# Optimization experiments

Hardware: AMD Instinct MI355X
Metric: run time of the kernel (lower is better)

The kernel has to match this reference:

```python
import jax, jax.numpy as jnp
import numpy as np

TOP_K = 2  # top-k experts per token


def setup_inputs() -> dict:
    key = jax.random.key(0)
    k1, k2, k3, k4, k5 = jax.random.split(key, 5)
    B, S, D = 1, 2048, 2048
    E, F = 8, 1408
    scale = 0.02
    return {
        "hidden_states": jax.random.normal(k1, (B, S, D), dtype=jnp.float32),
        "gate_w": jax.random.normal(k2, (E, D), dtype=jnp.float32) * scale,
        "w_gate": jax.random.normal(k3, (E, D, F), dtype=jnp.float32) * scale,
        "w_up": jax.random.normal(k4, (E, D, F), dtype=jnp.float32) * scale,
        "w_down": jax.random.normal(k5, (E, F, D), dtype=jnp.float32) * scale,
    }


def reference(hidden_states, gate_w, w_gate, w_up, w_down):
    B, S, D = hidden_states.shape
    T = B * S
    x = hidden_states.reshape(T, D)  # flatten tokens, as in forward()

    # Router: combined gate built from per-rank 1-row gates -> [T, E] logits
    router_logits = jnp.einsum("td,ed->te", x, gate_w)
    routing_weights = jax.nn.softmax(router_logits, axis=-1)
    top_w, top_idx = jax.lax.top_k(routing_weights, TOP_K)  # [T, K]

    # Per-token combine weight for each expert (0 if expert not selected).
    # Equivalent to the one_hot expert_mask + index_add combine in the module.
    comb = jnp.zeros((T, gate_w.shape[0]), dtype=routing_weights.dtype)
    comb = comb.at[jnp.arange(T)[:, None], top_idx].add(top_w)  # [T, E]

    # Each expert is a Qwen2 MLP: down(silu(gate(x)) * up(x)).
    # (Dispatch/all-to-all collapses to dense-per-expert + masked combine
    #  on a single device; tokens with comb==0 contribute nothing.)
    g = jnp.einsum("td,edf->etf", x, w_gate)
    u = jnp.einsum("td,edf->etf", x, w_up)
    y = jnp.einsum("etf,efd->etd", jax.nn.silu(g) * u, w_down)  # [E, T, D]

    out = jnp.einsum("te,etd->td", comb, y)  # weighted combine (index_add)
    return out.reshape(B, S, D)
```

## Files before the change

kernel.cpp:

```cpp
#include <hip/hip_runtime.h>
#include <stdint.h>


#define TT 2048
#define DD 2048
#define FF 1408
#define NE 8
#define HROWS 5120
#define TRASH (2*TT)

typedef float f32x4 __attribute__((ext_vector_type(4)));
typedef short bf16x8 __attribute__((ext_vector_type(8)));
typedef short bf16x4 __attribute__((ext_vector_type(4)));
typedef const __attribute__((address_space(3))) unsigned short* lds_cp;

__device__ __forceinline__ unsigned short f2bf(float f) {
    unsigned int x = __float_as_uint(f);
    return (unsigned short)((x + 0x7fffu + ((x >> 16) & 1u)) >> 16);
}
__device__ __forceinline__ float bf2f(unsigned short u) {
    union { unsigned int i; float f; } v; v.i = ((unsigned int)u) << 16; return v.f;
}
__device__ __forceinline__ void gld16(const void* g, void* l) {
    __builtin_amdgcn_global_load_lds((const __attribute__((address_space(1))) void*)g,
                                     (__attribute__((address_space(3))) void*)l, 16, 0, 0);
}

#define TR16(d, p, imm) \
    asm volatile("ds_read_b64_tr_b16 %0, %1 offset:" imm : "=&v"(d) : "v"(p))

__global__ void convert_gu_kernel(const float* __restrict__ wg,
                                  const float* __restrict__ wu,
                                  unsigned short* __restrict__ G,
                                  unsigned short* __restrict__ U) {
    const int z = blockIdx.z;
    const float* s; unsigned short* d;
    if (z < NE) { s = wg + (size_t)z * DD * FF;        d = G + (size_t)z * DD * FF; }
    else        { s = wu + (size_t)(z - NE) * DD * FF; d = U + (size_t)(z - NE) * DD * FF; }
    const size_t i = ((size_t)blockIdx.x * 256 + threadIdx.x) * 8;
    float4 a = *(const float4*)(s + i);
    float4 b = *(const float4*)(s + i + 4);
    uint4 o; unsigned short* po = (unsigned short*)&o;
    po[0] = f2bf(a.x); po[1] = f2bf(a.y); po[2] = f2bf(a.z); po[3] = f2bf(a.w);
    po[4] = f2bf(b.x); po[5] = f2bf(b.y); po[6] = f2bf(b.z); po[7] = f2bf(b.w);
    *(uint4*)(d + i) = o;
}

__global__ void convert_d_kernel(const float* __restrict__ wd,
                                 unsigned short* __restrict__ W) {
    const int z = blockIdx.z;
    const float* s = wd + (size_t)z * FF * DD;
    unsigned short* d = W + (size_t)z * FF * DD;
    const size_t i = ((size_t)blockIdx.x * 256 + threadIdx.x) * 8;
    float4 a = *(const float4*)(s + i);
    float4 b = *(const float4*)(s + i + 4);
    uint4 o; unsigned short* po = (unsigned short*)&o;
    po[0] = f2bf(a.x); po[1] = f2bf(a.y); po[2] = f2bf(a.z); po[3] = f2bf(a.w);
    po[4] = f2bf(b.x); po[5] = f2bf(b.y); po[6] = f2bf(b.z); po[7] = f2bf(b.w);
    *(uint4*)(d + i) = o;
}

__global__ void router_kernel(const float* __restrict__ x,
                              const float* __restrict__ gw,
                              int* __restrict__ cnt,
                              int* __restrict__ tok,
                              float* __restrict__ wtv,
                              int* __restrict__ dstv,
                              unsigned short* __restrict__ xb,
                              int* __restrict__ basep,
                              int* __restrict__ cntpad) {
    __shared__ int s_last;
    __shared__ int sc[NE], sp[NE];

    const int wv = threadIdx.x >> 6, lane = threadIdx.x & 63;
    const int t = blockIdx.x * 4 + wv;
    float acc[NE];
#pragma unroll
    for (int e = 0; e < NE; ++e) acc[e] = 0.f;
    const float* xr = x + (size_t)t * DD;
    unsigned short* xbr = xb + (size_t)t * DD;
#pragma unroll
    for (int it = 0; it < DD / 256; ++it) {
        const int j = it * 256 + lane * 4;
        float4 xv = *(const float4*)(xr + j);
        short4 o;
        o.x = (short)f2bf(xv.x); o.y = (short)f2bf(xv.y);
        o.z = (short)f2bf(xv.z); o.w = (short)f2bf(xv.w);
        *(short4*)(xbr + j) = o;
#pragma unroll
        for (int e = 0; e < NE; ++e) {
            float4 g = *(const float4*)(gw + e * DD + j);
            acc[e] += xv.x * g.x + xv.y * g.y + xv.z * g.z + xv.w * g.w;
        }
    }
#pragma unroll
    for (int e = 0; e < NE; ++e) {
        float v = acc[e];
        v += __shfl_xor(v, 32); v += __shfl_xor(v, 16); v += __shfl_xor(v, 8);
        v += __shfl_xor(v, 4);  v += __shfl_xor(v, 2);  v += __shfl_xor(v, 1);
        acc[e] = v;
    }
    if (lane == 0) {
        float mx = acc[0];
#pragma unroll
        for (int e = 1; e < NE; ++e) mx = fmaxf(mx, acc[e]);
        float p[NE], s = 0.f;
#pragma unroll
        for (int e = 0; e < NE; ++e) { p[e] = __expf(acc[e] - mx); s += p[e]; }
        int i0 = 0;
#pragma unroll
        for (int e = 1; e < NE; ++e) if (p[e] > p[i0]) i0 = e;
        int i1 = (i0 == 0) ? 1 : 0;
#pragma unroll
        for (int e = 0; e < NE; ++e) if (e != i0 && p[e] > p[i1]) i1 = e;
        float inv = 1.f / s;
        int p0 = atomicAdd(&cnt[i0], 1);
        tok[i0 * TT + p0] = t; wtv[i0 * TT + p0] = p[i0] * inv; dstv[i0 * TT + p0] = 2 * t;
        int p1 = atomicAdd(&cnt[i1], 1);
        tok[i1 * TT + p1] = t; wtv[i1 * TT + p1] = p[i1] * inv; dstv[i1 * TT + p1] = 2 * t + 1;
    }

    __syncthreads();
    if (threadIdx.x == 0) {
        __threadfence();
        int d = atomicAdd(&cnt[NE], 1);
        s_last = (d == (TT / 4) - 1) ? 1 : 0;
    }
    __syncthreads();
    if (s_last) {
        if (threadIdx.x == 0) {
            int b = 0;
            for (int e = 0; e < NE; ++e) {
                int c = atomicAdd(&cnt[e], 0);
                int pd = (c + 127) & ~127;
                basep[e] = b; cntpad[e] = pd; sc[e] = c; sp[e] = pd; b += pd;
            }
        }
        __syncthreads();
        for (int e = 0; e < NE; ++e)
            for (int i = sc[e] + (int)threadIdx.x; i < sp[e]; i += 256) {
                tok[e * TT + i] = 0; wtv[e * TT + i] = 0.f; dstv[e * TT + i] = TRASH;
            }
    }
}


__launch_bounds__(256, 2)
__global__ void gemm1_kernel(const unsigned short* __restrict__ Xb,
                             const unsigned short* __restrict__ Wg,
                             const unsigned short* __restrict__ Wu,
                             const int* __restrict__ tok,
                             const int* __restrict__ base,
                             const int* __restrict__ cntpad,
                             unsigned short* __restrict__ H) {
    __shared__ unsigned short As[128 * 32];
    __shared__ unsigned short Bg[128 * 32];
    __shared__ unsigned short Bu[128 * 32];
    __shared__ int s_tok[128];

    const int e = blockIdx.z, rb = blockIdx.y, fb = blockIdx.x;
    const int cp = cntpad[e];
    if (rb * 128 >= cp) return;
    const int b0 = base[e];

    const int tid = threadIdx.x;
    if (tid < 128) s_tok[tid] = tok[e * TT + rb * 128 + tid];
    __syncthreads();

    const int w = tid >> 6, lane = tid & 63;
    const int r = lane & 15, q = lane >> 4;
    const int wm = w & 1, wn = w >> 1;

    const int srow = w * 32 + (lane >> 2);
    const int koff = (lane & 3) * 8;
    const unsigned short* ga0 = Xb + (size_t)s_tok[srow] * DD + koff;
    const unsigned short* ga1 = Xb + (size_t)s_tok[srow + 16] * DD + koff;
    unsigned short* la0 = As + srow * 32 + koff;
    unsigned short* la1 = la0 + 512;

    const int s0 = tid, s1 = tid + 256;
    const int k0 = 4 * (s0 >> 6) + ((s0 >> 1) & 3), f0 = 16 * ((s0 >> 3) & 7) + 8 * (s0 & 1);
    const int k1 = 4 * (s1 >> 6) + ((s1 >> 1) & 3), f1 = 16 * ((s1 >> 3) & 7) + 8 * (s1 & 1);
    const size_t wb = (size_t)e * DD * FF + (size_t)fb * 128;
    const unsigned short* gg0 = Wg + wb + (size_t)k0 * FF + f0;
    const unsigned short* gg1 = Wg + wb + (size_t)k1 * FF + f1;
    const unsigned short* gu0 = Wu + wb + (size_t)k0 * FF + f0;
    const unsigned short* gu1 = Wu + wb + (size_t)k1 * FF + f1;
    unsigned short* lg0 = Bg + s0 * 8;
    unsigned short* lg1 = Bg + s1 * 8;
    unsigned short* lu0 = Bu + s0 * 8;
    unsigned short* lu1 = Bu + s1 * 8;

    lds_cp bg = (lds_cp)Bg + (q * 1024 + wn * 256 + 4 * r);
    lds_cp bu = (lds_cp)Bu + (q * 1024 + wn * 256 + 4 * r);

    f32x4 accg[4][4] = {};
    f32x4 accu[4][4] = {};

    for (int kt = 0; kt < DD / 32; ++kt) {
        gld16(ga0, la0); gld16(ga1, la1);
        gld16(gg0, lg0); gld16(gg1, lg1);
        gld16(gu0, lu0); gld16(gu1, lu1);
        ga0 += 32; ga1 += 32;
        gg0 += 32 * FF; gg1 += 32 * FF; gu0 += 32 * FF; gu1 += 32 * FF;
        __syncthreads();

        bf16x8 af[4];
#pragma unroll
        for (int m = 0; m < 4; ++m)
            af[m] = *(const bf16x8*)&As[(wm * 64 + m * 16 + r) * 32 + q * 8];

        bf16x4 gA[8], uA[8];
        TR16(gA[0], bg, "0");    TR16(gA[1], bg, "1024");
        TR16(gA[2], bg, "128");  TR16(gA[3], bg, "1152");
        TR16(gA[4], bg, "256");  TR16(gA[5], bg, "1280");
        TR16(gA[6], bg, "384");  TR16(gA[7], bg, "1408");
        TR16(uA[0], bu, "0");    TR16(uA[1], bu, "1024");
        TR16(uA[2], bu, "128");  TR16(uA[3], bu, "1152");
        TR16(uA[4], bu, "256");  TR16(uA[5], bu, "1280");
        TR16(uA[6], bu, "384");  TR16(uA[7], bu, "1408");
        asm volatile("s_waitcnt lgkmcnt(0)" ::: "memory");
        __builtin_amdgcn_sched_barrier(0);

        bf16x8 gf[4], uf[4];
#pragma unroll
        for (int n = 0; n < 4; ++n) {
            gf[n] = __builtin_shufflevector(gA[2 * n], gA[2 * n + 1], 0, 1, 2, 3, 4, 5, 6, 7);
            uf[n] = __builtin_shufflevector(uA[2 * n], uA[2 * n + 1], 0, 1, 2, 3, 4, 5, 6, 7);
        }
#pragma unroll
        for (int m = 0; m < 4; ++m)
#pragma unroll
            for (int n = 0; n < 4; ++n) {
                accg[m][n] = __builtin_amdgcn_mfma_f32_16x16x32_bf16(af[m], gf[n], accg[m][n], 0, 0, 0);
                accu[m][n] = __builtin_amdgcn_mfma_f32_16x16x32_bf16(af[m], uf[n], accu[m][n], 0, 0, 0);
            }
        __syncthreads();
    }

    const size_t hr0 = (size_t)(b0 + rb * 128 + wm * 64);
#pragma unroll
    for (int m = 0; m < 4; ++m)
#pragma unroll
        for (int n = 0; n < 4; ++n)
#pragma unroll
            for (int rr = 0; rr < 4; ++rr) {
                float g = accg[m][n][rr], u = accu[m][n][rr];
                float h = (g / (1.f + __expf(-g))) * u;
                int row = m * 16 + q * 4 + rr;
                int col = fb * 128 + wn * 64 + n * 16 + r;
                H[(hr0 + row) * FF + col] = f2bf(h);
            }
}

__launch_bounds__(256, 2)
__global__ void gemm2_kernel(const unsigned short* __restrict__ H,
                             const unsigned short* __restrict__ Wd,
                             const float* __restrict__ wtv,
                             const int* __restrict__ dstv,
                             const int* __restrict__ base,
                             const int* __restrict__ cntpad,
                             unsigned short* __restrict__ Y) {
    __shared__ unsigned short As[128 * 32];
    __shared__ unsigned short Bs[128 * 32];
    __shared__ float s_w[128];
    __shared__ int s_d[128];

    const int e = blockIdx.z, rb = blockIdx.y, db = blockIdx.x;
    const int cp = cntpad[e];
    if (rb * 128 >= cp) return;
    const int b0 = base[e];

    const int tid = threadIdx.x;
    if (tid < 128) {
        int idx = e * TT + rb * 128 + tid;
        s_w[tid] = wtv[idx]; s_d[tid] = dstv[idx];
    }
    __syncthreads();

    const int w = tid >> 6, lane = tid & 63;
    const int r = lane & 15, q = lane >> 4;
    const int wm = w & 1, wn = w >> 1;

    const int srow = w * 32 + (lane >> 2);
    const int koff = (lane & 3) * 8;
    const unsigned short* ga0 = H + (size_t)(b0 + rb * 128 + srow) * FF + koff;
    const unsigned short* ga1 = ga0 + (size_t)16 * FF;
    unsigned short* la0 = As + srow * 32 + koff;
    unsigned short* la1 = la0 + 512;

    const int s0 = tid, s1 = tid + 256;
    const int k0 = 4 * (s0 >> 6) + ((s0 >> 1) & 3), f0 = 16 * ((s0 >> 3) & 7) + 8 * (s0 & 1);
    const int k1 = 4 * (s1 >> 6) + ((s1 >> 1) & 3), f1 = 16 * ((s1 >> 3) & 7) + 8 * (s1 & 1);
    const size_t wb = (size_t)e * FF * DD + (size_t)db * 128;
    const unsigned short* gb0 = Wd + wb + (size_t)k0 * DD + f0;
    const unsigned short* gb1 = Wd + wb + (size_t)k1 * DD + f1;
    unsigned short* lb0 = Bs + s0 * 8;
    unsigned short* lb1 = Bs + s1 * 8;

    lds_cp bb = (lds_cp)Bs + (q * 1024 + wn * 256 + 4 * r);

    f32x4 acc[4][4] = {};

    for (int kt = 0; kt < FF / 32; ++kt) {
        gld16(ga0, la0); gld16(ga1, la1);
        gld16(gb0, lb0); gld16(gb1, lb1);
        ga0 += 32; ga1 += 32;
        gb0 += 32 * DD; gb1 += 32 * DD;
        __syncthreads();

        bf16x8 af[4];
#pragma unroll
        for (int m = 0; m < 4; ++m)
            af[m] = *(const bf16x8*)&As[(wm * 64 + m * 16 + r) * 32 + q * 8];

        bf16x4 bA[8];
        TR16(bA[0], bb, "0");    TR16(bA[1], bb, "1024");
        TR16(bA[2], bb, "128");  TR16(bA[3], bb, "1152");
        TR16(bA[4], bb, "256");  TR16(bA[5], bb, "1280");
        TR16(bA[6], bb, "384");  TR16(bA[7], bb, "1408");
        asm volatile("s_waitcnt lgkmcnt(0)" ::: "memory");
        __builtin_amdgcn_sched_barrier(0);

        bf16x8 bf[4];
#pragma unroll
        for (int n = 0; n < 4; ++n)
            bf[n] = __builtin_shufflevector(bA[2 * n], bA[2 * n + 1], 0, 1, 2, 3, 4, 5, 6, 7);
#pragma unroll
        for (int m = 0; m < 4; ++m)
#pragma unroll
            for (int n = 0; n < 4; ++n)
                acc[m][n] = __builtin_amdgcn_mfma_f32_16x16x32_bf16(af[m], bf[n], acc[m][n], 0, 0, 0);
        __syncthreads();
    }

#pragma unroll
    for (int m = 0; m < 4; ++m)
#pragma unroll
        for (int n = 0; n < 4; ++n)
#pragma unroll
            for (int rr = 0; rr < 4; ++rr) {
                int row = wm * 64 + m * 16 + q * 4 + rr;
                int col = db * 128 + wn * 64 + n * 16 + r;
                float v = s_w[row] * acc[m][n][rr];
                Y[(size_t)s_d[row] * DD + col] = f2bf(v);
            }
}

__global__ void combine_kernel(const unsigned short* __restrict__ Y,
                               float* __restrict__ out) {
    const int t = blockIdx.x;
    const int d = threadIdx.x * 8;
    uint4 a = *(const uint4*)(Y + (size_t)(2 * t) * DD + d);
    uint4 b = *(const uint4*)(Y + (size_t)(2 * t + 1) * DD + d);
    const unsigned short* pa = (const unsigned short*)&a;
    const unsigned short* pb = (const unsigned short*)&b;
    float4 o0, o1;
    o0.x = bf2f(pa[0]) + bf2f(pb[0]);  o0.y = bf2f(pa[1]) + bf2f(pb[1]);
    o0.z = bf2f(pa[2]) + bf2f(pb[2]);  o0.w = bf2f(pa[3]) + bf2f(pb[3]);
    o1.x = bf2f(pa[4]) + bf2f(pb[4]);  o1.y = bf2f(pa[5]) + bf2f(pb[5]);
    o1.z = bf2f(pa[6]) + bf2f(pb[6]);  o1.w = bf2f(pa[7]) + bf2f(pb[7]);
    float* op = out + (size_t)t * DD + d;
    ((float4*)op)[0] = o0;
    ((float4*)op)[1] = o1;
}

extern "C" void kernel_launch(void* const* d_in, const int* in_sizes, int n_in,
                              void* d_out, int out_size, void* d_ws, size_t ws_size,
                              hipStream_t stream) {
    const float* x      = (const float*)d_in[0];
    const float* gw     = (const float*)d_in[1];
    const float* w_gate = (const float*)d_in[2];
    const float* w_up   = (const float*)d_in[3];
    const float* w_down = (const float*)d_in[4];
    float* out = (float*)d_out;

    uint8_t* ws = (uint8_t*)d_ws;
    size_t off = 0;
    auto alloc = [&](size_t bytes) -> void* {
        void* p = ws + off;
        off = (off + bytes + 255) & ~(size_t)255;
        return p;
    };
    int*   cnt    = (int*)  alloc((NE + 1) * 4);
    int*   basep  = (int*)  alloc(NE * 4);
    int*   cntpad = (int*)  alloc(NE * 4);
    int*   tok    = (int*)  alloc((size_t)NE * TT * 4);
    float* wtv    = (float*)alloc((size_t)NE * TT * 4);
    int*   dstv   = (int*)  alloc((size_t)NE * TT * 4);
    unsigned short* Xb  = (unsigned short*)alloc((size_t)TT * DD * 2);
    unsigned short* Hb  = (unsigned short*)alloc((size_t)HROWS * FF * 2);
    unsigned short* Yb  = (unsigned short*)alloc((size_t)(2 * TT + 8) * DD * 2);
    unsigned short* WT  = (unsigned short*)alloc((size_t)2 * NE * FF * DD * 2);
    unsigned short* WgB = WT;
    unsigned short* WuB = WT + (size_t)NE * FF * DD;
    unsigned short* WdB = WT;
    (void)ws_size; (void)in_sizes; (void)n_in; (void)out_size;

    hipMemsetAsync(cnt, 0, (NE + 1) * 4, stream);
    convert_gu_kernel<<<dim3(DD * FF / 2048, 1, 2 * NE), 256, 0, stream>>>(w_gate, w_up, WgB, WuB);
    router_kernel<<<dim3(TT / 4), 256, 0, stream>>>(x, gw, cnt, tok, wtv, dstv, Xb, basep, cntpad);
    gemm1_kernel<<<dim3(FF / 128, TT / 128, NE), 256, 0, stream>>>(Xb, WgB, WuB, tok, basep, cntpad, Hb);
    convert_d_kernel<<<dim3(FF * DD / 2048, 1, NE), 256, 0, stream>>>(w_down, WdB);
    gemm2_kernel<<<dim3(DD / 128, TT / 128, NE), 256, 0, stream>>>(Hb, WdB, wtv, dstv, basep, cntpad, Yb);
    combine_kernel<<<dim3(TT), 256, 0, stream>>>(Yb, out);
}
```

Measured before the change: 497.6 us.

## Double-buffer LDS tiles in both expert GEMMs and remap block order

Both grouped GEMM kernels now keep two LDS buffers and issue the next K-tile's global-to-LDS loads before computing on the current one. Explicit vmcnt waits and raw s_barrier calls replace the per-iteration __syncthreads, so memory latency can overlap the MFMA work. Block indices are also permuted so that consecutively launched blocks are spread across row and column tiles, which changes how weight tiles are reused in cache. LDS use per block doubles, which could reduce occupancy, and the hand-written wait counts must match the number of loads in flight or the results will be wrong.

Result: slower. 666.9 us (+34.0%).

```diff
diff --git a/kernel.cpp b/kernel.cpp
--- a/kernel.cpp
+++ b/kernel.cpp
@@ -28,6 +28,9 @@
 
 #define TR16(d, p, imm) \
     asm volatile("ds_read_b64_tr_b16 %0, %1 offset:" imm : "=&v"(d) : "v"(p))
+
+#define WAITV(n)  asm volatile("s_waitcnt vmcnt(" #n ")" ::: "memory")
+#define BARRIER() asm volatile("s_barrier" ::: "memory")
 
 __global__ void convert_gu_kernel(const float* __restrict__ wg,
                                   const float* __restrict__ wu,
@@ -144,6 +147,50 @@
     }
 }
 
+#define G1_STAGE(BUF) do {                                                     \
+    gld16(ga0, &As[BUF][a_s0]); gld16(ga1, &As[BUF][a_s1]);                    \
+    gld16(gg0, &Bg[BUF][b_s0]); gld16(gg1, &Bg[BUF][b_s1]);                    \
+    gld16(gu0, &Bu[BUF][b_s0]); gld16(gu1, &Bu[BUF][b_s1]);                    \
+    ga0 += 32; ga1 += 32;                                                      \
+    gg0 += 32 * FF; gg1 += 32 * FF; gu0 += 32 * FF; gu1 += 32 * FF;            \
+} while (0)
+
+#define G1_COMPUTE(BUF) do {                                                   \
+    bf16x8 af[4];                                                              \
+    af[0] = *(const bf16x8*)&As[BUF][ar0];                                     \
+    af[1] = *(const bf16x8*)&As[BUF][ar0 + 512];                               \
+    af[2] = *(const bf16x8*)&As[BUF][ar0 + 1024];                              \
+    af[3] = *(const bf16x8*)&As[BUF][ar0 + 1536];                              \
+    bf16x4 gA[8], uA[8];                                                       \
+    {                                                                          \
+        lds_cp bgp = (lds_cp)(&Bg[BUF][0]) + boff;                             \
+        lds_cp bup = (lds_cp)(&Bu[BUF][0]) + boff;                             \
+        TR16(gA[0], bgp, "0");    TR16(gA[1], bgp, "1024");                    \
+        TR16(gA[2], bgp, "128");  TR16(gA[3], bgp, "1152");                    \
+        TR16(gA[4], bgp, "256");  TR16(gA[5], bgp, "1280");                    \
+        TR16(gA[6], bgp, "384");  TR16(gA[7], bgp, "1408");                    \
+        TR16(uA[0], bup, "0");    TR16(uA[1], bup, "1024");                    \
+        TR16(uA[2], bup, "128");  TR16(uA[3], bup, "1152");                    \
+        TR16(uA[4], bup, "256");  TR16(uA[5], bup, "1280");                    \
+        TR16(uA[6], bup, "384");  TR16(uA[7], bup, "1408");                    \
+    }                                                                          \
+    asm volatile("s_waitcnt lgkmcnt(0)" ::: "memory");                         \
+    __builtin_amdgcn_sched_barrier(0);                                         \
+    bf16x8 gf[4], uf[4];                                                       \
+    _Pragma("unroll")                                                          \
+    for (int n = 0; n < 4; ++n) {                                              \
+        gf[n] = __builtin_shufflevector(gA[2*n], gA[2*n+1], 0,1,2,3,4,5,6,7);  \
+        uf[n] = __builtin_shufflevector(uA[2*n], uA[2*n+1], 0,1,2,3,4,5,6,7);  \
+    }                                                                          \
+    _Pragma("unroll")                                                          \
+    for (int m = 0; m < 4; ++m) {                                              \
+        _Pragma("unroll")                                                      \
+        for (int n = 0; n < 4; ++n) {                                          \
+            accg[m][n] = __builtin_amdgcn_mfma_f32_16x16x32_bf16(af[m], gf[n], accg[m][n], 0, 0, 0); \
+            accu[m][n] = __builtin_amdgcn_mfma_f32_16x16x32_bf16(af[m], uf[n], accu[m][n], 0, 0, 0); \
+        }                                                                      \
+    }                                                                          \
+} while (0)
 
 __launch_bounds__(256, 2)
 __global__ void gemm1_kernel(const unsigned short* __restrict__ Xb,
@@ -153,12 +200,16 @@
                              const int* __restrict__ base,
                              const int* __restrict__ cntpad,
                              unsigned short* __restrict__ H) {
-    __shared__ unsigned short As[128 * 32];
-    __shared__ unsigned short Bg[128 * 32];
-    __shared__ unsigned short Bu[128 * 32];
+    __shared__ unsigned short As[2][128 * 32];
+    __shared__ unsigned short Bg[2][128 * 32];
+    __shared__ unsigned short Bu[2][128 * 32];
     __shared__ int s_tok[128];
 
-    const int e = blockIdx.z, rb = blockIdx.y, fb = blockIdx.x;
+    const int e = blockIdx.z;
+    const int u = blockIdx.y * 11 + blockIdx.x;
+    const int wk = 22 * (u & 7) + (u >> 3);
+    const int rb = wk / 11, fb = wk % 11;
+
     const int cp = cntpad[e];
     if (rb * 128 >= cp) return;
     const int b0 = base[e];
@@ -175,8 +226,7 @@
     const int koff = (lane & 3) * 8;
     const unsigned short* ga0 = Xb + (size_t)s_tok[srow] * DD + koff;
     const unsigned short* ga1 = Xb + (size_t)s_tok[srow + 16] * DD + koff;
-    unsigned short* la0 = As + srow * 32 + koff;
-    unsigned short* la1 = la0 + 512;
+    const int a_s0 = srow * 32 + koff, a_s1 = a_s0 + 512;
 
     const int s0 = tid, s1 = tid + 256;
     const int k0 = 4 * (s0 >> 6) + ((s0 >> 1) & 3), f0 = 16 * ((s0 >> 3) & 7) + 8 * (s0 & 1);
@@ -186,56 +236,30 @@
     const unsigned short* gg1 = Wg + wb + (size_t)k1 * FF + f1;
     const unsigned short* gu0 = Wu + wb + (size_t)k0 * FF + f0;
     const unsigned short* gu1 = Wu + wb + (size_t)k1 * FF + f1;
-    unsigned short* lg0 = Bg + s0 * 8;
-    unsigned short* lg1 = Bg + s1 * 8;
-    unsigned short* lu0 = Bu + s0 * 8;
-    unsigned short* lu1 = Bu + s1 * 8;
-
-    lds_cp bg = (lds_cp)Bg + (q * 1024 + wn * 256 + 4 * r);
-    lds_cp bu = (lds_cp)Bu + (q * 1024 + wn * 256 + 4 * r);
+    const int b_s0 = s0 * 8, b_s1 = s1 * 8;
+
+    const int ar0 = (wm * 64 + r) * 32 + q * 8;
+    const int boff = q * 1024 + wn * 256 + 4 * r;
 
     f32x4 accg[4][4] = {};
     f32x4 accu[4][4] = {};
 
-    for (int kt = 0; kt < DD / 32; ++kt) {
-        gld16(ga0, la0); gld16(ga1, la1);
-        gld16(gg0, lg0); gld16(gg1, lg1);
-        gld16(gu0, lu0); gld16(gu1, lu1);
-        ga0 += 32; ga1 += 32;
-        gg0 += 32 * FF; gg1 += 32 * FF; gu0 += 32 * FF; gu1 += 32 * FF;
-        __syncthreads();
-
-        bf16x8 af[4];
-#pragma unroll
-        for (int m = 0; m < 4; ++m)
-            af[m] = *(const bf16x8*)&As[(wm * 64 + m * 16 + r) * 32 + q * 8];
-
-        bf16x4 gA[8], uA[8];
-        TR16(gA[0], bg, "0");    TR16(gA[1], bg, "1024");
-        TR16(gA[2], bg, "128");  TR16(gA[3], bg, "1152");
-        TR16(gA[4], bg, "256");  TR16(gA[5], bg, "1280");
-        TR16(gA[6], bg, "384");  TR16(gA[7], bg, "1408");
-        TR16(uA[0], bu, "0");    TR16(uA[1], bu, "1024");
-        TR16(uA[2], bu, "128");  TR16(uA[3], bu, "1152");
-        TR16(uA[4], bu, "256");  TR16(uA[5], bu, "1280");
-        TR16(uA[6], bu, "384");  TR16(uA[7], bu, "1408");
-        asm volatile("s_waitcnt lgkmcnt(0)" ::: "memory");
-        __builtin_amdgcn_sched_barrier(0);
-
-        bf16x8 gf[4], uf[4];
-#pragma unroll
-        for (int n = 0; n < 4; ++n) {
-            gf[n] = __builtin_shufflevector(gA[2 * n], gA[2 * n + 1], 0, 1, 2, 3, 4, 5, 6, 7);
-            uf[n] = __builtin_shufflevector(uA[2 * n], uA[2 * n + 1], 0, 1, 2, 3, 4, 5, 6, 7);
+    G1_STAGE(0);
+    for (int kt = 0; kt < DD / 32; kt += 2) {
+        G1_STAGE(1);
+        WAITV(6);
+        BARRIER();
+        G1_COMPUTE(0);
+        BARRIER();
+        if (kt + 2 < DD / 32) {
+            G1_STAGE(0);
+            WAITV(6);
+        } else {
+            WAITV(0);
         }
-#pragma unroll
-        for (int m = 0; m < 4; ++m)
-#pragma unroll
-            for (int n = 0; n < 4; ++n) {
-                accg[m][n] = __builtin_amdgcn_mfma_f32_16x16x32_bf16(af[m], gf[n], accg[m][n], 0, 0, 0);
-                accu[m][n] = __builtin_amdgcn_mfma_f32_16x16x32_bf16(af[m], uf[n], accu[m][n], 0, 0, 0);
-            }
-        __syncthreads();
+        BARRIER();
+        G1_COMPUTE(1);
+        BARRIER();
     }
 
     const size_t hr0 = (size_t)(b0 + rb * 128 + wm * 64);
@@ -245,13 +269,47 @@
         for (int n = 0; n < 4; ++n)
 #pragma unroll
             for (int rr = 0; rr < 4; ++rr) {
-                float g = accg[m][n][rr], u = accu[m][n][rr];
-                float h = (g / (1.f + __expf(-g))) * u;
+                float g = accg[m][n][rr], u2 = accu[m][n][rr];
+                float h = (g / (1.f + __expf(-g))) * u2;
                 int row = m * 16 + q * 4 + rr;
                 int col = fb * 128 + wn * 64 + n * 16 + r;
                 H[(hr0 + row) * FF + col] = f2bf(h);
             }
 }
+
+#define G2_STAGE(BUF) do {                                                     \
+    gld16(ga0, &As[BUF][a_s0]); gld16(ga1, &As[BUF][a_s1]);                    \
+    gld16(gb0, &Bs[BUF][b_s0]); gld16(gb1, &Bs[BUF][b_s1]);                    \
+    ga0 += 32; ga1 += 32; gb0 += 32 * DD; gb1 += 32 * DD;                      \
+} while (0)
+
+#define G2_COMPUTE(BUF) do {                                                   \
+    bf16x8 af[4];                                                              \
+    af[0] = *(const bf16x8*)&As[BUF][ar0];                                     \
+    af[1] = *(const bf16x8*)&As[BUF][ar0 + 512];                               \
+    af[2] = *(const bf16x8*)&As[BUF][ar0 + 1024];                              \
+    af[3] = *(const bf16x8*)&As[BUF][ar0 + 1536];                              \
+    bf16x4 bA[8];                                                              \
+    {                                                                          \
+        lds_cp bbp = (lds_cp)(&Bs[BUF][0]) + boff;                             \
+        TR16(bA[0], bbp, "0");    TR16(bA[1], bbp, "1024");                    \
+        TR16(bA[2], bbp, "128");  TR16(bA[3], bbp, "1152");                    \
+        TR16(bA[4], bbp, "256");  TR16(bA[5], bbp, "1280");                    \
+        TR16(bA[6], bbp, "384");  TR16(bA[7], bbp, "1408");                    \
+    }                                                                          \
+    asm volatile("s_waitcnt lgkmcnt(0)" ::: "memory");                         \
+    __builtin_amdgcn_sched_barrier(0);                                         \
+    bf16x8 bfv[4];                                                             \
+    _Pragma("unroll")                                                          \
+    for (int n = 0; n < 4; ++n)                                                \
+        bfv[n] = __builtin_shufflevector(bA[2*n], bA[2*n+1], 0,1,2,3,4,5,6,7); \
+    _Pragma("unroll")                                                          \
+    for (int m = 0; m < 4; ++m) {                                              \
+        _Pragma("unroll")                                                      \
+        for (int n = 0; n < 4; ++n)                                            \
+            acc[m][n] = __builtin_amdgcn_mfma_f32_16x16x32_bf16(af[m], bfv[n], acc[m][n], 0, 0, 0); \
+    }                                                                          \
+} while (0)
 
 __launch_bounds__(256, 2)
 __global__ void gemm2_kernel(const unsigned short* __restrict__ H,
@@ -261,12 +319,16 @@
                              const int* __restrict__ base,
                              const int* __restrict__ cntpad,
                              unsigned short* __restrict__ Y) {
-    __shared__ unsigned short As[128 * 32];
-    __shared__ unsigned short Bs[128 * 32];
+    __shared__ unsigned short As[2][128 * 32];
+    __shared__ unsigned short Bs[2][128 * 32];
     __shared__ float s_w[128];
     __shared__ int s_d[128];
 
-    const int e = blockIdx.z, rb = blockIdx.y, db = blockIdx.x;
+    const int e = blockIdx.z;
+    const int u = blockIdx.y * 16 + blockIdx.x;
+    const int wk = 32 * (u & 7) + (u >> 3);
+    const int rb = wk >> 4, db = wk & 15;
+
     const int cp = cntpad[e];
     if (rb * 128 >= cp) return;
     const int b0 = base[e];
@@ -286,8 +348,7 @@
     const int koff = (lane & 3) * 8;
     const unsigned short* ga0 = H + (size_t)(b0 + rb * 128 + srow) * FF + koff;
     const unsigned short* ga1 = ga0 + (size_t)16 * FF;
-    unsigned short* la0 = As + srow * 32 + koff;
-    unsigned short* la1 = la0 + 512;
+    const int a_s0 = srow * 32 + koff, a_s1 = a_s0 + 512;
 
     const int s0 = tid, s1 = tid + 256;
     const int k0 = 4 * (s0 >> 6) + ((s0 >> 1) & 3), f0 = 16 * ((s0 >> 3) & 7) + 8 * (s0 & 1);
@@ -295,43 +356,29 @@
     const size_t wb = (size_t)e * FF * DD + (size_t)db * 128;
     const unsigned short* gb0 = Wd + wb + (size_t)k0 * DD + f0;
     const unsigned short* gb1 = Wd + wb + (size_t)k1 * DD + f1;
-    unsigned short* lb0 = Bs + s0 * 8;
-    unsigned short* lb1 = Bs + s1 * 8;
-
-    lds_cp bb = (lds_cp)Bs + (q * 1024 + wn * 256 + 4 * r);
+    const int b_s0 = s0 * 8, b_s1 = s1 * 8;
+
+    const int ar0 = (wm * 64 + r) * 32 + q * 8;
+    const int boff = q * 1024 + wn * 256 + 4 * r;
 
     f32x4 acc[4][4] = {};
 
-    for (int kt = 0; kt < FF / 32; ++kt) {
-        gld16(ga0, la0); gld16(ga1, la1);
-        gld16(gb0, lb0); gld16(gb1, lb1);
-        ga0 += 32; ga1 += 32;
-        gb0 += 32 * DD; gb1 += 32 * DD;
-        __syncthreads();
-
-        bf16x8 af[4];
-#pragma unroll
-        for (int m = 0; m < 4; ++m)
-            af[m] = *(const bf16x8*)&As[(wm * 64 + m * 16 + r) * 32 + q * 8];
-
-        bf16x4 bA[8];
-        TR16(bA[0], bb, "0");    TR16(bA[1], bb, "1024");
-        TR16(bA[2], bb, "128");  TR16(bA[3], bb, "1152");
-        TR16(bA[4], bb, "256");  TR16(bA[5], bb, "1280");
-        TR16(bA[6], bb, "384");  TR16(bA[7], bb, "1408");
-        asm volatile("s_waitcnt lgkmcnt(0)" ::: "memory");
-        __builtin_amdgcn_sched_barrier(0);
-
-        bf16x8 bf[4];
-#pragma unroll
-        for (int n = 0; n < 4; ++n)
-            bf[n] = __builtin_shufflevector(bA[2 * n], bA[2 * n + 1], 0, 1, 2, 3, 4, 5, 6, 7);
-#pragma unroll
-        for (int m = 0; m < 4; ++m)
-#pragma unroll
-            for (int n = 0; n < 4; ++n)
-                acc[m][n] = __builtin_amdgcn_mfma_f32_16x16x32_bf16(af[m], bf[n], acc[m][n], 0, 0, 0);
-        __syncthreads();
+    G2_STAGE(0);
+    for (int kt = 0; kt < FF / 32; kt += 2) {
+        G2_STAGE(1);
+        WAITV(4);
+        BARRIER();
+        G2_COMPUTE(0);
+        BARRIER();
+        if (kt + 2 < FF / 32) {
+            G2_STAGE(0);
+            WAITV(4);
+        } else {
+            WAITV(0);
+        }
+        BARRIER();
+        G2_COMPUTE(1);
+        BARRIER();
     }
 
 #pragma unroll
```
